# Optimization experiments

Measured on AMD Instinct MI355X. Metric: run time of the kernel, lower is better.

## Reference

```python
import jax, jax.numpy as jnp
import numpy as np

B, N, HW, PS, FHW = 16, 4096, 224, 8, 56

def _gelu(x):
    return jax.nn.gelu(x, approximate=True)  # tanh approximation, matches nn.GELU(approximate='tanh')

def _conv(x, w, b, stride):
    y = jax.lax.conv_general_dilated(x, w, (stride, stride), [(1, 1), (1, 1)],
                                     dimension_numbers=('NCHW', 'OIHW', 'NCHW'))
    return y + b[None, :, None, None]

def _embed(points):
    # for i in 0..11: append sin(2^i * p) then cos(2^i * p) -> [B,N,48]
    factors = 2.0 ** jnp.arange(12, dtype=points.dtype)
    scaled = points[..., None, :] * factors[:, None]          # [B,N,12,2]
    feats = jnp.concatenate([jnp.sin(scaled), jnp.cos(scaled)], axis=-1)  # [B,N,12,4]
    return feats.reshape(points.shape[0], points.shape[1], 48)

def _extract_patches(fmap, points):
    # fmap [B,C,H,W]; points in [0,1]; bilinear grid_sample, zeros padding, align_corners=True
    Bq, C, H, W = fmap.shape
    centers = points * 2.0 - 1.0
    step = 2.0 / (W - 1)
    half = (PS - 1) / 2.0
    offs = jnp.linspace(-half, half, PS, dtype=fmap.dtype) * step
    offx2d, offy2d = jnp.meshgrid(offs, offs, indexing='ij')   # [ps,ps]
    gx = centers[..., 0][..., None, None] + offx2d             # [B,N,ps,ps]
    gy = centers[..., 1][..., None, None] + offy2d
    # align_corners=True pixel coords
    ix = (gx + 1.0) * 0.5 * (W - 1)
    iy = (gy + 1.0) * 0.5 * (H - 1)
    x0f = jnp.floor(ix); y0f = jnp.floor(iy)
    x0 = x0f.astype(jnp.int32); y0 = y0f.astype(jnp.int32)
    x1 = x0 + 1; y1 = y0 + 1
    wx1 = ix - x0f; wx0 = 1.0 - wx1
    wy1 = iy - y0f; wy0 = 1.0 - wy1
    fflat = fmap.reshape(Bq, C, H * W)

    def corner(xi, yi, w):
        valid = ((xi >= 0) & (xi < W) & (yi >= 0) & (yi < H)).astype(fmap.dtype)
        idx = jnp.clip(yi, 0, H - 1) * W + jnp.clip(xi, 0, W - 1)   # [B,N,ps,ps]
        vals = jax.vmap(lambda f, i: f[:, i])(fflat, idx)           # [B,C,N,ps,ps]
        return vals * (w * valid)[:, None]

    out = (corner(x0, y0, wx0 * wy0) + corner(x1, y0, wx1 * wy0)
           + corner(x0, y1, wx0 * wy1) + corner(x1, y1, wx1 * wy1))  # [B,C,N,ps,ps]
    return out.transpose(0, 2, 1, 3, 4)                              # [B,N,C,ps,ps]

def setup_inputs():
    key = jax.random.key(0)
    ks = jax.random.split(key, 26)
    def w(k, shape):
        fan_in = int(np.prod(shape[1:]))
        return jax.random.normal(k, shape, jnp.float32) * (1.0 / np.sqrt(fan_in))
    inp = {
        'points': jax.random.uniform(ks[0], (B, N, 2), jnp.float32),
        'images': jax.random.normal(ks[1], (B, 3, HW, HW), jnp.float32),
        # plane encoder
        'pw1': w(ks[2], (16, 3, 3, 3)),  'pb1': jnp.zeros((16,), jnp.float32),
        'pw2': w(ks[3], (32, 16, 3, 3)), 'pb2': jnp.zeros((32,), jnp.float32),
        'pw3': w(ks[4], (4, 32, 3, 3)),  'pb3': jnp.zeros((4,), jnp.float32),
        # global encoder
        'gw1': w(ks[5], (4, 3, 3, 3)),   'gb1': jnp.zeros((4,), jnp.float32),
        'gw2': w(ks[6], (8, 4, 3, 3)),   'gb2': jnp.zeros((8,), jnp.float32),
        'gw3': w(ks[7], (16, 8, 3, 3)),  'gb3': jnp.zeros((16,), jnp.float32),
        'gw4': w(ks[8], (32, 16, 3, 3)), 'gb4': jnp.zeros((32,), jnp.float32),
        'gw5': w(ks[9], (64, 32, 3, 3)), 'gb5': jnp.zeros((64,), jnp.float32),
        # point encoder (torch Linear: [out,in])
        'lw1': w(ks[10], (256, 48)),  'lb1': jnp.zeros((256,), jnp.float32),
        'lw2': w(ks[11], (256, 256)), 'lb2': jnp.zeros((256,), jnp.float32),
        # head
        'hw1': w(ks[12], (512, 576)), 'hb1': jnp.zeros((512,), jnp.float32),
        'hw2': w(ks[13], (1, 512)),   'hb2': jnp.zeros((1,), jnp.float32),
    }
    return inp

def reference(points, images, pw1, pb1, pw2, pb2, pw3, pb3,
              gw1, gb1, gw2, gb2, gw3, gb3, gw4, gb4, gw5, gb5,
              lw1, lb1, lw2, lb2, hw1, hb1, hw2, hb2):
    # point branch
    pe = _embed(points)                                         # [B,N,48]
    pf = _gelu(pe @ lw1.T + lb1) @ lw2.T + lb2                  # [B,N,256]
    # plane encoder -> 4x56x56 fmap
    f = _gelu(_conv(images, pw1, pb1, 2))
    f = _gelu(_conv(f, pw2, pb2, 2))
    fmap = _gelu(_conv(f, pw3, pb3, 1))                         # [B,4,56,56]
    # global encoder -> [B,64]
    g = images
    for wg, bg in ((gw1, gb1), (gw2, gb2), (gw3, gb3), (gw4, gb4), (gw5, gb5)):
        g = _gelu(_conv(g, wg, bg, 2))
    gc = g.mean(axis=(2, 3))                                    # AvgPool2d(7)+Flatten -> [B,64]
    gc = jnp.broadcast_to(gc[:, None, :], (points.shape[0], points.shape[1], 64))
    # per-point bilinear patch gather
    patches = _extract_patches(fmap, points).reshape(points.shape[0], points.shape[1], -1)  # [B,N,256]
    fused = jnp.concatenate([pf, patches, gc], axis=-1)         # [B,N,576]
    logit = _gelu(fused @ hw1.T + hb1) @ hw2.T + hb2            # [B,N,1]
    return logit
```

## Files before the change

kernel.cpp:

```cpp
#include <hip/hip_runtime.h>
#include <math.h>

#define BB 16
#define NN 4096
#define M_TOT (BB*NN)
#define TBK 32

typedef __attribute__((ext_vector_type(8))) short s8v;
typedef __attribute__((ext_vector_type(4))) float f4v;

__device__ __forceinline__ float gelu_t(float x){
    float u = 1.5957691216057308f * x * (1.0f + 0.044715f*x*x);
    return x / (1.0f + __expf(-u));
}

__device__ __forceinline__ unsigned short f2bf(float f){
    unsigned int u = __float_as_uint(f);
    u += 0x7fffu + ((u >> 16) & 1u);
    return (unsigned short)(u >> 16);
}

#define GLL(src, dst) __builtin_amdgcn_global_load_lds( \
    (const __attribute__((address_space(1))) void*)(src), \
    (__attribute__((address_space(3))) void*)(dst), 16, 0, 0)

template<int CIN, int COUT, int STRIDE>
__device__ __forceinline__ void conv_dev(
    const float* __restrict__ in, const float* __restrict__ w,
    const float* __restrict__ bias, float* __restrict__ out,
    int Hin, int Win, int Hout, int Wout, int bx, int by, int b, float* tile)
{
    constexpr int IW = 15*STRIDE + 3;
    constexpr int IH = IW;
    int tid = threadIdx.x;
    int tx = tid & 15, ty = tid >> 4;
    int wo = bx*16 + tx;
    int ho = by*16 + ty;
    int win0 = bx*16*STRIDE - 1;
    int hin0 = by*16*STRIDE - 1;
    bool valid = (wo < Wout) && (ho < Hout);

    float acc[COUT];
    #pragma unroll
    for (int co = 0; co < COUT; ++co) acc[co] = bias[co];

    const float* ib = in + (size_t)(b*CIN)*Hin*Win;
    for (int ci = 0; ci < CIN; ++ci) {
        __syncthreads();
        const float* ic = ib + (size_t)ci*Hin*Win;
        for (int idx = tid; idx < IH*IW; idx += 256) {
            int r = idx / IW, c = idx - r*IW;
            int hi = hin0 + r, wi = win0 + c;
            float v = 0.f;
            if ((unsigned)hi < (unsigned)Hin && (unsigned)wi < (unsigned)Win)
                v = ic[hi*Win + wi];
            tile[r*34 + c] = v;
        }
        __syncthreads();
        float vv[9];
        #pragma unroll
        for (int kh = 0; kh < 3; ++kh)
            #pragma unroll
            for (int kw = 0; kw < 3; ++kw)
                vv[kh*3+kw] = tile[(ty*STRIDE + kh)*34 + tx*STRIDE + kw];
        const float* wc = w + ci*9;
        #pragma unroll
        for (int co = 0; co < COUT; ++co) {
            const float* wp = wc + co*CIN*9;
            #pragma unroll
            for (int k = 0; k < 9; ++k)
                acc[co] = fmaf(vv[k], wp[k], acc[co]);
        }
    }
    if (valid) {
        size_t obase = ((size_t)b*COUT)*Hout*Wout + (size_t)ho*Wout + wo;
        #pragma unroll
        for (int co = 0; co < COUT; ++co)
            out[obase + (size_t)co*Hout*Wout] = gelu_t(acc[co]);
    }
}

__device__ __forceinline__ void conv_p3_dev(
    const float* __restrict__ in, const float* __restrict__ w,
    const float* __restrict__ bias, float4* __restrict__ out,
    int bx, int by, int b, float* tile)
{
    int tid = threadIdx.x;
    int tx = tid & 15, ty = tid >> 4;
    int wo = bx*16 + tx;
    int ho = by*16 + ty;
    int win0 = bx*16 - 1;
    int hin0 = by*16 - 1;
    bool valid = (ho < 56) && (wo < 56);

    float acc[4];
    #pragma unroll
    for (int co = 0; co < 4; ++co) acc[co] = bias[co];

    const float* ib = in + (size_t)(b*32)*3136;
    for (int ci = 0; ci < 32; ++ci) {
        __syncthreads();
        const float* ic = ib + (size_t)ci*3136;
        for (int idx = tid; idx < 18*18; idx += 256) {
            int r = idx / 18, c = idx - r*18;
            int hi = hin0 + r, wi = win0 + c;
            float v = 0.f;
            if ((unsigned)hi < 56u && (unsigned)wi < 56u)
                v = ic[hi*56 + wi];
            tile[r*34 + c] = v;
        }
        __syncthreads();
        float vv[9];
        #pragma unroll
        for (int kh = 0; kh < 3; ++kh)
            #pragma unroll
            for (int kw = 0; kw < 3; ++kw)
                vv[kh*3+kw] = tile[(ty + kh)*34 + tx + kw];
        #pragma unroll
        for (int co = 0; co < 4; ++co) {
            const float* wp = w + co*288 + ci*9;
            #pragma unroll
            for (int k = 0; k < 9; ++k)
                acc[co] = fmaf(vv[k], wp[k], acc[co]);
        }
    }
    if (valid) {
        float4 o;
        o.x = gelu_t(acc[0]); o.y = gelu_t(acc[1]);
        o.z = gelu_t(acc[2]); o.w = gelu_t(acc[3]);
        out[(size_t)b*3136 + (size_t)ho*56 + wo] = o;
    }
}

__global__ __launch_bounds__(256) void conv_dual_k(
    const float* __restrict__ in,
    const float* __restrict__ wA, const float* __restrict__ bA,
    const float* __restrict__ wB, const float* __restrict__ bB,
    float* __restrict__ outA, float* __restrict__ outB)
{
    constexpr int IW = 33, IH = 33;
    const int Hin = 224, Win = 224, Hout = 112, Wout = 112;
    __shared__ float tile[IH][IW + 1];
    int tid = threadIdx.x;
    int tx = tid & 15, ty = tid >> 4;
    int b = blockIdx.z;
    int wo = blockIdx.x*16 + tx;
    int ho = blockIdx.y*16 + ty;
    int win0 = blockIdx.x*32 - 1;
    int hin0 = blockIdx.y*32 - 1;

    float accA[16], accB[4];
    #pragma unroll
    for (int co = 0; co < 16; ++co) accA[co] = bA[co];
    #pragma unroll
    for (int co = 0; co < 4; ++co) accB[co] = bB[co];

    const float* ib = in + (size_t)(b*3)*Hin*Win;
    for (int ci = 0; ci < 3; ++ci) {
        __syncthreads();
        const float* ic = ib + (size_t)ci*Hin*Win;
        for (int idx = tid; idx < IH*IW; idx += 256) {
            int r = idx / IW, c = idx - r*IW;
            int hi = hin0 + r, wi = win0 + c;
            float v = 0.f;
            if ((unsigned)hi < (unsigned)Hin && (unsigned)wi < (unsigned)Win)
                v = ic[hi*Win + wi];
            tile[r][c] = v;
        }
        __syncthreads();
        float vv[9];
        #pragma unroll
        for (int kh = 0; kh < 3; ++kh)
            #pragma unroll
            for (int kw = 0; kw < 3; ++kw)
                vv[kh*3+kw] = tile[ty*2 + kh][tx*2 + kw];
        #pragma unroll
        for (int co = 0; co < 16; ++co) {
            const float* wp = wA + co*27 + ci*9;
            #pragma unroll
            for (int k = 0; k < 9; ++k) accA[co] = fmaf(vv[k], wp[k], accA[co]);
        }
        #pragma unroll
        for (int co = 0; co < 4; ++co) {
            const float* wp = wB + co*27 + ci*9;
            #pragma unroll
            for (int k = 0; k < 9; ++k) accB[co] = fmaf(vv[k], wp[k], accB[co]);
        }
    }
    size_t px = (size_t)ho*Wout + wo;
    #pragma unroll
    for (int co = 0; co < 16; ++co)
        outA[((size_t)(b*16 + co))*Hout*Wout + px] = gelu_t(accA[co]);
    #pragma unroll
    for (int co = 0; co < 4; ++co)
        outB[((size_t)(b*4 + co))*Hout*Wout + px] = gelu_t(accB[co]);
}

__global__ __launch_bounds__(256) void conv_pg2_k(
    const float* __restrict__ f1, const float* __restrict__ pw2, const float* __restrict__ pb2, float* __restrict__ f2,
    const float* __restrict__ g1, const float* __restrict__ gw2, const float* __restrict__ gb2, float* __restrict__ g2)
{
    __shared__ float tile[33*34];
    int z = blockIdx.z;
    if (z < 16) conv_dev<16,32,2>(f1, pw2, pb2, f2, 112,112, 56,56, blockIdx.x, blockIdx.y, z, tile);
    else        conv_dev<4,8,2> (g1, gw2, gb2, g2, 112,112, 56,56, blockIdx.x, blockIdx.y, z-16, tile);
}

__global__ __launch_bounds__(256) void conv_pg3_k(
    const float* __restrict__ f2, const float* __restrict__ pw3, const float* __restrict__ pb3, float4* __restrict__ fmap4,
    const float* __restrict__ g2, const float* __restrict__ gw3, const float* __restrict__ gb3, float* __restrict__ g3)
{
    __shared__ float tile[33*34];
    int z = blockIdx.z;
    if (z < 16) {
        conv_p3_dev(f2, pw3, pb3, fmap4, blockIdx.x, blockIdx.y, z, tile);
    } else {
        if (blockIdx.x >= 2 || blockIdx.y >= 2) return;
        conv_dev<8,16,2>(g2, gw3, gb3, g3, 56,56, 28,28, blockIdx.x, blockIdx.y, z-16, tile);
    }
}

__global__ __launch_bounds__(256) void tail_k(
    const float* __restrict__ g3, const float* __restrict__ w4, const float* __restrict__ b4,
    const float* __restrict__ w5, const float* __restrict__ b5, float* __restrict__ gc)
{
    __shared__ float s3[16*784];
    __shared__ float s4[32*196];
    __shared__ float s5[64*49];
    int b = blockIdx.x, tid = threadIdx.x;
    const float* src = g3 + (size_t)b*16*784;
    for (int i = tid; i < 16*784; i += 256) s3[i] = src[i];
    __syncthreads();
    if (tid < 196) {
        int ho = tid/14, wo = tid - (tid/14)*14;
        float acc[32];
        #pragma unroll
        for (int co = 0; co < 32; ++co) acc[co] = b4[co];
        for (int ci = 0; ci < 16; ++ci) {
            #pragma unroll
            for (int kh = 0; kh < 3; ++kh) {
                int hi = ho*2 - 1 + kh;
                if ((unsigned)hi >= 28u) continue;
                #pragma unroll
                for (int kw = 0; kw < 3; ++kw) {
                    int wi = wo*2 - 1 + kw;
                    if ((unsigned)wi >= 28u) continue;
                    float v = s3[ci*784 + hi*28 + wi];
                    int wofs = ci*9 + kh*3 + kw;
                    #pragma unroll
                    for (int co = 0; co < 32; ++co)
                        acc[co] = fmaf(v, w4[co*144 + wofs], acc[co]);
                }
            }
        }
        #pragma unroll
        for (int co = 0; co < 32; ++co) s4[co*196 + tid] = gelu_t(acc[co]);
    }
    __syncthreads();
    if (tid < 196) {
        int px = tid % 49, cg = tid / 49;
        int ho = px/7, wo = px - (px/7)*7;
        float acc[16];
        #pragma unroll
        for (int c = 0; c < 16; ++c) acc[c] = b5[cg*16 + c];
        for (int ci = 0; ci < 32; ++ci) {
            #pragma unroll
            for (int kh = 0; kh < 3; ++kh) {
                int hi = ho*2 - 1 + kh;
                if ((unsigned)hi >= 14u) continue;
                #pragma unroll
                for (int kw = 0; kw < 3; ++kw) {
                    int wi = wo*2 - 1 + kw;
                    if ((unsigned)wi >= 14u) continue;
                    float v = s4[ci*196 + hi*14 + wi];
                    int wofs = ci*9 + kh*3 + kw;
                    #pragma unroll
                    for (int c = 0; c < 16; ++c)
                        acc[c] = fmaf(v, w5[(cg*16 + c)*288 + wofs], acc[c]);
                }
            }
        }
        #pragma unroll
        for (int c = 0; c < 16; ++c) s5[(cg*16 + c)*49 + px] = gelu_t(acc[c]);
    }
    __syncthreads();
    if (tid < 64) {
        float s = 0.f;
        #pragma unroll
        for (int k = 0; k < 49; ++k) s += s5[tid*49 + k];
        gc[b*64 + tid] = s * (1.0f/49.0f);
    }
}

__global__ void cvtall_k(const float* __restrict__ lw1, const float* __restrict__ lw2,
                         const float* __restrict__ hw1, unsigned short* __restrict__ blw1,
                         unsigned short* __restrict__ blw2, unsigned short* __restrict__ bhw1){
    int i = blockIdx.x*blockDim.x + threadIdx.x;
    if (i < 256*64) {
        int r = i >> 6, c = i & 63;
        blw1[i] = (c < 48) ? f2bf(lw1[r*48 + c]) : 0;
        return;
    }
    i -= 256*64;
    if (i < 256*256) { blw2[i] = f2bf(lw2[i]); return; }
    i -= 256*256;
    if (i < 512*576) bhw1[i] = f2bf(hw1[i]);
}

__global__ __launch_bounds__(512) void mlp12_k(
    const float* __restrict__ points,
    const unsigned short* __restrict__ W1, const float* __restrict__ b1,
    const unsigned short* __restrict__ W2, const float* __restrict__ b2,
    unsigned short* __restrict__ C,
    const float4* __restrict__ fmap4, const float* __restrict__ gc)
{
    __shared__ unsigned short Hd[128*256];
    __shared__ unsigned short B2[256*TBK];
    int tid = threadIdx.x;
    int wv = tid >> 6, lane = tid & 63;
    int q = lane >> 4, lr = lane & 15;
    int mi = wv >> 2, ni = wv & 3;
    size_t m0 = (size_t)blockIdx.x * 128;

    f4v acc1[4][4];
    #pragma unroll
    for (int i = 0; i < 4; ++i)
        #pragma unroll
        for (int j = 0; j < 4; ++j) acc1[i][j] = (f4v){0.f,0.f,0.f,0.f};

    #pragma unroll
    for (int kb = 0; kb < 2; ++kb) {
        int seg = kb*4 + q;
        s8v a[4], b[4];
        #pragma unroll
        for (int t = 0; t < 4; ++t) {
            size_t m = m0 + mi*64 + t*16 + lr;
            float px = points[m*2], py = points[m*2+1];
            union { s8v v; unsigned short u[8]; } pk;
            #pragma unroll
            for (int j = 0; j < 8; ++j) {
                int k = seg*8 + j;
                unsigned short val = 0;
                if (k < 48) {
                    int i2 = k >> 2, rr = k & 3;
                    float f = (float)(1 << i2);
                    float p = (rr & 1) ? py : px;
                    float s = f * p;
                    val = f2bf((rr < 2) ? __sinf(s) : __cosf(s));
                }
                pk.u[j] = val;
            }
            a[t] = pk.v;
        }
        #pragma unroll
        for (int t = 0; t < 4; ++t) {
            int n = ni*64 + t*16 + lr;
            b[t] = *(const s8v*)(W1 + n*64 + seg*8);
        }
        #pragma unroll
        for (int mt = 0; mt < 4; ++mt)
            #pragma unroll
            for (int nt = 0; nt < 4; ++nt)
                acc1[mt][nt] = __builtin_amdgcn_mfma_f32_16x16x32_bf16(a[mt], b[nt], acc1[mt][nt], 0, 0, 0);
    }
    {
        float b1v[4];
        #pragma unroll
        for (int nt = 0; nt < 4; ++nt) b1v[nt] = b1[ni*64 + nt*16 + lr];
        #pragma unroll
        for (int mt = 0; mt < 4; ++mt)
            #pragma unroll
            for (int r4 = 0; r4 < 4; ++r4) {
                int row = mi*64 + mt*16 + q*4 + r4;
                #pragma unroll
                for (int nt = 0; nt < 4; ++nt) {
                    int col = ni*64 + nt*16 + lr;
                    float v = gelu_t(acc1[mt][nt][r4] + b1v[nt]);
                    int p = (col >> 3) ^ (row & 7);
                    Hd[(row*32 + p)*8 + (col & 7)] = f2bf(v);
                }
            }
    }
    __syncthreads();

    f4v acc2[4][4];
    #pragma unroll
    for (int i = 0; i < 4; ++i)
        #pragma unroll
        for (int j = 0; j < 4; ++j) acc2[i][j] = (f4v){0.f,0.f,0.f,0.f};

    for (int kt = 0; kt < 8; ++kt) {
        #pragma unroll
        for (int r = 0; r < 2; ++r) {
            int f = r*512 + tid;
            int rr = f >> 2, ll = (f & 3) ^ ((f >> 3) & 3);
            GLL(W2 + rr*256 + kt*32 + ll*8, B2 + f*8);
        }
        __syncthreads();
        s8v a[4], b[4];
        int sw = q ^ ((lr >> 1) & 3);
        #pragma unroll
        for (int t = 0; t < 4; ++t) {
            int row = mi*64 + t*16 + lr;
            int p = (kt*4 + q) ^ (row & 7);
            a[t] = *(const s8v*)(Hd + (row*32 + p)*8);
        }
        #pragma unroll
        for (int t = 0; t < 4; ++t) {
            int n = ni*64 + t*16 + lr;
            b[t] = *(const s8v*)(B2 + (n*4 + sw)*8);
        }
        #pragma unroll
        for (int mt = 0; mt < 4; ++mt)
            #pragma unroll
            for (int nt = 0; nt < 4; ++nt)
                acc2[mt][nt] = __builtin_amdgcn_mfma_f32_16x16x32_bf16(a[mt], b[nt], acc2[mt][nt], 0, 0, 0);
        __syncthreads();
    }
    {
        float b2v[4];
        #pragma unroll
        for (int nt = 0; nt < 4; ++nt) b2v[nt] = b2[ni*64 + nt*16 + lr];
        #pragma unroll
        for (int mt = 0; mt < 4; ++mt)
            #pragma unroll
            for (int r4 = 0; r4 < 4; ++r4) {
                size_t m = m0 + mi*64 + mt*16 + q*4 + r4;
                #pragma unroll
                for (int nt = 0; nt < 4; ++nt) {
                    int n = ni*64 + nt*16 + lr;
                    C[m*576 + n] = f2bf(acc2[mt][nt][r4] + b2v[nt]);
                }
            }
    }
    #pragma unroll 1
    for (int it = 0; it < 16; ++it) {
        int task = it*512 + tid;
        int ml = task >> 6, ij = task & 63;
        size_t m = m0 + ml;
        int i = ij >> 3, j = ij & 7;
        int b = (int)(m >> 12);
        float px = points[m*2], py = points[m*2+1];
        float cx = px*2.f - 1.f, cy = py*2.f - 1.f;
        const float step = 2.0f/55.0f;
        float gx = cx + ((float)i - 3.5f)*step;
        float gy = cy + ((float)j - 3.5f)*step;
        float ix = (gx + 1.f)*0.5f*55.f;
        float iy = (gy + 1.f)*0.5f*55.f;
        float x0f = floorf(ix), y0f = floorf(iy);
        int x0 = (int)x0f, y0 = (int)y0f;
        int x1 = x0 + 1,  y1 = y0 + 1;
        float wx1 = ix - x0f, wx0 = 1.f - wx1;
        float wy1 = iy - y0f, wy0 = 1.f - wy1;
        float v00 = ((x0>=0)&&(x0<56)&&(y0>=0)&&(y0<56)) ? 1.f : 0.f;
        float v10 = ((x1>=0)&&(x1<56)&&(y0>=0)&&(y0<56)) ? 1.f : 0.f;
        float v01 = ((x0>=0)&&(x0<56)&&(y1>=0)&&(y1<56)) ? 1.f : 0.f;
        float v11 = ((x1>=0)&&(x1<56)&&(y1>=0)&&(y1<56)) ? 1.f : 0.f;
        float w00 = wx0*wy0*v00, w10 = wx1*wy0*v10, w01 = wx0*wy1*v01, w11 = wx1*wy1*v11;
        int cx0 = min(max(x0,0),55), cx1 = min(max(x1,0),55);
        int cy0 = min(max(y0,0),55), cy1 = min(max(y1,0),55);
        const float4* fb = fmap4 + (size_t)b*3136;
        float4 f00 = fb[cy0*56 + cx0], f10 = fb[cy0*56 + cx1];
        float4 f01 = fb[cy1*56 + cx0], f11 = fb[cy1*56 + cx1];
        float4 v;
        v.x = w00*f00.x + w10*f10.x + w01*f01.x + w11*f11.x;
        v.y = w00*f00.y + w10*f10.y + w01*f01.y + w11*f11.y;
        v.z = w00*f00.z + w10*f10.z + w01*f01.z + w11*f11.z;
        v.w = w00*f00.w + w10*f10.w + w01*f01.w + w11*f11.w;
        C[m*576 + 256 +   0 + ij] = f2bf(v.x);
        C[m*576 + 256 +  64 + ij] = f2bf(v.y);
        C[m*576 + 256 + 128 + ij] = f2bf(v.z);
        C[m*576 + 256 + 192 + ij] = f2bf(v.w);
        C[m*576 + 512 + ij] = f2bf(gc[b*64 + ij]);
    }
}

__global__ __launch_bounds__(512) void gemm_hd_k(
    const unsigned short* __restrict__ A,
    const unsigned short* __restrict__ W,
    const float* __restrict__ bias, const float* __restrict__ w2,
    const float* __restrict__ b2, float* __restrict__ out)
{
    __shared__ unsigned short Bs[512*TBK];
    __shared__ float red[8*64];
    int tid = threadIdx.x;
    int wv = tid >> 6, lane = tid & 63;
    int q = lane >> 4, lr = lane & 15;
    int sw = q ^ ((lr >> 1) & 3);
    int ms = wv >> 2, nb = (wv & 3) * 128;
    size_t m0 = (size_t)blockIdx.x * 128;

    const unsigned short* srcB[4]; unsigned short* dstB[4];
    #pragma unroll
    for (int r = 0; r < 4; ++r) {
        int f = r*512 + tid;
        int rr = f >> 2, ll = (f & 3) ^ ((rr >> 1) & 3);
        srcB[r] = W + (size_t)rr*576 + ll*8;
        dstB[r] = Bs + f*8;
    }
    const unsigned short* Arow[4];
    #pragma unroll
    for (int t = 0; t < 4; ++t)
        Arow[t] = A + (m0 + ms*64 + t*16 + lr)*576 + q*8;

    f4v acc[4][8];
    #pragma unroll
    for (int i = 0; i < 4; ++i)
        #pragma unroll
        for (int j = 0; j < 8; ++j) acc[i][j] = (f4v){0.f,0.f,0.f,0.f};

    for (int k0 = 0; k0 < 576; k0 += TBK) {
        #pragma unroll
        for (int r = 0; r < 4; ++r) { GLL(srcB[r], dstB[r]); srcB[r] += TBK; }
        s8v a[4];
        #pragma unroll
        for (int t = 0; t < 4; ++t) { a[t] = *(const s8v*)(Arow[t]); Arow[t] += TBK; }
        __syncthreads();
        s8v b[8];
        #pragma unroll
        for (int t = 0; t < 8; ++t)
            b[t] = *(const s8v*)(Bs + (nb + t*16 + lr)*TBK + sw*8);
        #pragma unroll
        for (int mt = 0; mt < 4; ++mt)
            #pragma unroll
            for (int nt = 0; nt < 8; ++nt)
                acc[mt][nt] = __builtin_amdgcn_mfma_f32_16x16x32_bf16(a[mt], b[nt], acc[mt][nt], 0, 0, 0);
        __syncthreads();
    }
    float bv[8], w2v[8];
    #pragma unroll
    for (int nt = 0; nt < 8; ++nt) {
        int n = nb + nt*16 + lr;
        bv[nt] = bias[n];
        w2v[nt] = w2[n];
    }
    #pragma unroll
    for (int mt = 0; mt < 4; ++mt)
        #pragma unroll
        for (int r4 = 0; r4 < 4; ++r4) {
            int ml = mt*16 + q*4 + r4;
            float s = 0.f;
            #pragma unroll
            for (int nt = 0; nt < 8; ++nt)
                s += gelu_t(acc[mt][nt][r4] + bv[nt]) * w2v[nt];
            #pragma unroll
            for (int off = 8; off > 0; off >>= 1) s += __shfl_down(s, off, 16);
            if (lr == 0) red[wv*64 + ml] = s;
        }
    __syncthreads();
    if (tid < 128) {
        int msf = tid >> 6, ml = tid & 63;
        float t = red[(msf*4+0)*64 + ml] + red[(msf*4+1)*64 + ml]
                + red[(msf*4+2)*64 + ml] + red[(msf*4+3)*64 + ml];
        out[blockIdx.x*128 + tid] = t + b2[0];
    }
}

extern "C" void kernel_launch(void* const* d_in, const int* in_sizes, int n_in,
                              void* d_out, int out_size, void* d_ws, size_t ws_size,
                              hipStream_t stream) {
    const float* points = (const float*)d_in[0];
    const float* images = (const float*)d_in[1];
    const float* pw1 = (const float*)d_in[2];  const float* pb1 = (const float*)d_in[3];
    const float* pw2 = (const float*)d_in[4];  const float* pb2 = (const float*)d_in[5];
    const float* pw3 = (const float*)d_in[6];  const float* pb3 = (const float*)d_in[7];
    const float* gw1 = (const float*)d_in[8];  const float* gb1 = (const float*)d_in[9];
    const float* gw2 = (const float*)d_in[10]; const float* gb2 = (const float*)d_in[11];
    const float* gw3 = (const float*)d_in[12]; const float* gb3 = (const float*)d_in[13];
    const float* gw4 = (const float*)d_in[14]; const float* gb4 = (const float*)d_in[15];
    const float* gw5 = (const float*)d_in[16]; const float* gb5 = (const float*)d_in[17];
    const float* lw1 = (const float*)d_in[18]; const float* lb1 = (const float*)d_in[19];
    const float* lw2 = (const float*)d_in[20]; const float* lb2 = (const float*)d_in[21];
    const float* hw1 = (const float*)d_in[22]; const float* hb1 = (const float*)d_in[23];
    const float* hw2 = (const float*)d_in[24]; const float* hb2 = (const float*)d_in[25];
    float* out = (float*)d_out;

    char* base = (char*)d_ws;
    unsigned short* fused_b = (unsigned short*)base;
    unsigned short* hid_b   = fused_b + (size_t)M_TOT*576;
    float4* fmap4 = (float4*)(hid_b + (size_t)M_TOT*256);
    float* gc   = (float*)(fmap4 + (size_t)16*3136);
    unsigned short* blw1 = (unsigned short*)(gc + 1024);
    unsigned short* blw2 = blw1 + 256*64;
    unsigned short* bhw1 = blw2 + 256*256;
    float* ct = (float*)base;
    float* f1 = ct;
    float* f2 = f1 + (size_t)16*16*112*112;
    float* g1 = f2 + (size_t)16*32*56*56;
    float* g2 = g1 + (size_t)16*4*112*112;
    float* g3 = g2 + (size_t)16*8*56*56;

    cvtall_k<<<1472, 256, 0, stream>>>(lw1, lw2, hw1, blw1, blw2, bhw1);
    conv_dual_k<<<dim3(7,7,16), 256, 0, stream>>>(images, pw1, pb1, gw1, gb1, f1, g1);
    conv_pg2_k<<<dim3(4,4,32), 256, 0, stream>>>(f1, pw2, pb2, f2, g1, gw2, gb2, g2);
    conv_pg3_k<<<dim3(4,4,32), 256, 0, stream>>>(f2, pw3, pb3, fmap4, g2, gw3, gb3, g3);
    tail_k<<<16, 256, 0, stream>>>(g3, gw4, gb4, gw5, gb5, gc);
    mlp12_k<<<M_TOT/128, 512, 0, stream>>>(points, blw1, lb1, blw2, lb2, fused_b, fmap4, gc);
    gemm_hd_k<<<M_TOT/128, 512, 0, stream>>>(fused_b, bhw1, hb1, hw2, hb2, out);
}
```

Baseline: 468.5 us.

## Split global-encoder tail into separate conv4, conv5 and avgpool kernels

The single per-batch tail kernel, which ran conv4, conv5 and the average pool in 16 blocks, is replaced by three kernels. Conv4 and conv5 now use flat per-pixel thread mappings with their weights staged in shared memory, and intermediates go through global buffers. Conv5 is now split into two 32-channel groups per pixel instead of four 16-channel groups. The aim is to cut the serial latency of the tail, where only a few threads per block were busy and weights came straight from global memory. The cost is two extra launches, a global round trip for g4 and g5, and very small grids (13, 7 and 4 blocks).

```diff
diff --git a/kernel.cpp b/kernel.cpp
--- a/kernel.cpp
+++ b/kernel.cpp
@@ -220,76 +220,95 @@
     }
 }
 
-__global__ __launch_bounds__(256) void tail_k(
-    const float* __restrict__ g3, const float* __restrict__ w4, const float* __restrict__ b4,
-    const float* __restrict__ w5, const float* __restrict__ b5, float* __restrict__ gc)
-{
-    __shared__ float s3[16*784];
-    __shared__ float s4[32*196];
-    __shared__ float s5[64*49];
-    int b = blockIdx.x, tid = threadIdx.x;
+__global__ __launch_bounds__(256) void g4_k(
+    const float* __restrict__ g3, const float* __restrict__ w4,
+    const float* __restrict__ b4, float* __restrict__ g4)
+{
+    __shared__ float ws[32*144];
+    int tid = threadIdx.x;
+    for (int i = tid; i < 32*144; i += 256) ws[i] = w4[i];
+    __syncthreads();
+    int idx = blockIdx.x*256 + tid;
+    if (idx >= 16*196) return;
+    int b = idx / 196, px = idx - (idx/196)*196;
+    int ho = px / 14, wo = px - (px/14)*14;
     const float* src = g3 + (size_t)b*16*784;
-    for (int i = tid; i < 16*784; i += 256) s3[i] = src[i];
+    float acc[32];
+    #pragma unroll
+    for (int co = 0; co < 32; ++co) acc[co] = b4[co];
+    for (int ci = 0; ci < 16; ++ci) {
+        #pragma unroll
+        for (int kh = 0; kh < 3; ++kh) {
+            int hi = ho*2 - 1 + kh;
+            if ((unsigned)hi >= 28u) continue;
+            #pragma unroll
+            for (int kw = 0; kw < 3; ++kw) {
+                int wi = wo*2 - 1 + kw;
+                if ((unsigned)wi >= 28u) continue;
+                float v = src[ci*784 + hi*28 + wi];
+                int wofs = ci*9 + kh*3 + kw;
+                #pragma unroll
+                for (int co = 0; co < 32; ++co)
+                    acc[co] = fmaf(v, ws[co*144 + wofs], acc[co]);
+            }
+        }
+    }
+    size_t obase = (size_t)b*32*196 + px;
+    #pragma unroll
+    for (int co = 0; co < 32; ++co)
+        g4[obase + (size_t)co*196] = gelu_t(acc[co]);
+}
+
+__global__ __launch_bounds__(256) void g5_k(
+    const float* __restrict__ g4, const float* __restrict__ w5,
+    const float* __restrict__ b5, float* __restrict__ g5)
+{
+    __shared__ float ws[64*288];
+    int tid = threadIdx.x;
+    for (int i = tid; i < 64*288; i += 256) ws[i] = w5[i];
     __syncthreads();
-    if (tid < 196) {
-        int ho = tid/14, wo = tid - (tid/14)*14;
-        float acc[32];
-        #pragma unroll
-        for (int co = 0; co < 32; ++co) acc[co] = b4[co];
-        for (int ci = 0; ci < 16; ++ci) {
-            #pragma unroll
-            for (int kh = 0; kh < 3; ++kh) {
-                int hi = ho*2 - 1 + kh;
-                if ((unsigned)hi >= 28u) continue;
+    int idx = blockIdx.x*256 + tid;
+    if (idx >= 16*49*2) return;
+    int cg = idx & 1;
+    int t = idx >> 1;
+    int b = t / 49, px = t - (t/49)*49;
+    int ho = px / 7, wo = px - (px/7)*7;
+    const float* src = g4 + (size_t)b*32*196;
+    const float* wsb = ws + cg*32*288;
+    float acc[32];
+    #pragma unroll
+    for (int c = 0; c < 32; ++c) acc[c] = b5[cg*32 + c];
+    for (int ci = 0; ci < 32; ++ci) {
+        #pragma unroll
+        for (int kh = 0; kh < 3; ++kh) {
+            int hi = ho*2 - 1 + kh;
+            if ((unsigned)hi >= 14u) continue;
+            #pragma unroll
+            for (int kw = 0; kw < 3; ++kw) {
+                int wi = wo*2 - 1 + kw;
+                if ((unsigned)wi >= 14u) continue;
+                float v = src[ci*196 + hi*14 + wi];
+                int wofs = ci*9 + kh*3 + kw;
                 #pragma unroll
-                for (int kw = 0; kw < 3; ++kw) {
-                    int wi = wo*2 - 1 + kw;
-                    if ((unsigned)wi >= 28u) continue;
-                    float v = s3[ci*784 + hi*28 + wi];
-                    int wofs = ci*9 + kh*3 + kw;
-                    #pragma unroll
-                    for (int co = 0; co < 32; ++co)
-                        acc[co] = fmaf(v, w4[co*144 + wofs], acc[co]);
-                }
+                for (int c = 0; c < 32; ++c)
+                    acc[c] = fmaf(v, wsb[c*288 + wofs], acc[c]);
             }
         }
-        #pragma unroll
-        for (int co = 0; co < 32; ++co) s4[co*196 + tid] = gelu_t(acc[co]);
-    }
-    __syncthreads();
-    if (tid < 196) {
-        int px = tid % 49, cg = tid / 49;
-        int ho = px/7, wo = px - (px/7)*7;
-        float acc[16];
-        #pragma unroll
-        for (int c = 0; c < 16; ++c) acc[c] = b5[cg*16 + c];
-        for (int ci = 0; ci < 32; ++ci) {
-            #pragma unroll
-            for (int kh = 0; kh < 3; ++kh) {
-                int hi = ho*2 - 1 + kh;
-                if ((unsigned)hi >= 14u) continue;
-                #pragma unroll
-                for (int kw = 0; kw < 3; ++kw) {
-                    int wi = wo*2 - 1 + kw;
-                    if ((unsigned)wi >= 14u) continue;
-                    float v = s4[ci*196 + hi*14 + wi];
-                    int wofs = ci*9 + kh*3 + kw;
-                    #pragma unroll
-                    for (int c = 0; c < 16; ++c)
-                        acc[c] = fmaf(v, w5[(cg*16 + c)*288 + wofs], acc[c]);
-                }
-            }
-        }
-        #pragma unroll
-        for (int c = 0; c < 16; ++c) s5[(cg*16 + c)*49 + px] = gelu_t(acc[c]);
-    }
-    __syncthreads();
-    if (tid < 64) {
-        float s = 0.f;
-        #pragma unroll
-        for (int k = 0; k < 49; ++k) s += s5[tid*49 + k];
-        gc[b*64 + tid] = s * (1.0f/49.0f);
-    }
+    }
+    size_t obase = (size_t)b*64*49 + (size_t)cg*32*49 + px;
+    #pragma unroll
+    for (int c = 0; c < 32; ++c)
+        g5[obase + (size_t)c*49] = gelu_t(acc[c]);
+}
+
+__global__ void avgpool7_k(const float* __restrict__ in, float* __restrict__ out){
+    int i = blockIdx.x*blockDim.x + threadIdx.x;
+    if (i >= BB*64) return;
+    const float* p = in + (size_t)i*49;
+    float s = 0.f;
+    #pragma unroll
+    for (int k = 0; k < 49; ++k) s += p[k];
+    out[i] = s * (1.0f/49.0f);
 }
 
 __global__ void cvtall_k(const float* __restrict__ lw1, const float* __restrict__ lw2,
@@ -589,12 +608,16 @@
     float* g1 = f2 + (size_t)16*32*56*56;
     float* g2 = g1 + (size_t)16*4*112*112;
     float* g3 = g2 + (size_t)16*8*56*56;
+    float* g4 = g3 + (size_t)16*16*28*28;
+    float* g5 = g4 + (size_t)16*32*14*14;
 
     cvtall_k<<<1472, 256, 0, stream>>>(lw1, lw2, hw1, blw1, blw2, bhw1);
     conv_dual_k<<<dim3(7,7,16), 256, 0, stream>>>(images, pw1, pb1, gw1, gb1, f1, g1);
     conv_pg2_k<<<dim3(4,4,32), 256, 0, stream>>>(f1, pw2, pb2, f2, g1, gw2, gb2, g2);
     conv_pg3_k<<<dim3(4,4,32), 256, 0, stream>>>(f2, pw3, pb3, fmap4, g2, gw3, gb3, g3);
-    tail_k<<<16, 256, 0, stream>>>(g3, gw4, gb4, gw5, gb5, gc);
+    g4_k<<<13, 256, 0, stream>>>(g3, gw4, gb4, g4);
+    g5_k<<<7, 256, 0, stream>>>(g4, gw5, gb5, g5);
+    avgpool7_k<<<4, 256, 0, stream>>>(g5, gc);
     mlp12_k<<<M_TOT/128, 512, 0, stream>>>(points, blw1, lb1, blw2, lb2, fused_b, fmap4, gc);
     gemm_hd_k<<<M_TOT/128, 512, 0, stream>>>(fused_b, bhw1, hb1, hw2, hb2, out);
 }
```

After: 493.8 us. 5.4% more time.
